# Performance work log

Hardware: AMD Instinct MI355X
Metric: run time of the kernel (lower is better)

Reference implementation:

```python
import jax, jax.numpy as jnp
import numpy as np

N_NODES = 50000
N_EDGES = 800000
D_IN, D_HID, D_OUT = 64, 128, 64


def _graph_conv(x, src, dst, w_rel, w_root, b):
    # PyG GraphConv with aggr='sum':
    #   out_i = W_rel @ sum_{j in N(i)} x_j + W_root @ x_i + b
    # Aggregate first at input width (sum commutes with the linear map),
    # then apply the two linear transforms.
    agg = jax.ops.segment_sum(x[src], dst, num_segments=x.shape[0])  # [N, d_in]
    return agg @ w_rel + x @ w_root + b


def setup_inputs() -> dict:
    key = jax.random.key(0)
    ks = jax.random.split(key, 9)
    x = jax.random.normal(ks[0], (N_NODES, D_IN), dtype=jnp.float32)
    edge_index = jax.random.randint(ks[1], (2, N_EDGES), 0, N_NODES, dtype=jnp.int64)

    def glorot(k, fan_in, fan_out):
        s = jnp.sqrt(2.0 / (fan_in + fan_out)).astype(jnp.float32)
        return jax.random.normal(k, (fan_in, fan_out), dtype=jnp.float32) * s

    return {
        "x": x,
        "edge_index": edge_index,
        "w_rel1": glorot(ks[2], D_IN, D_HID),  "w_root1": glorot(ks[3], D_IN, D_HID),  "b1": jnp.zeros((D_HID,), jnp.float32),
        "w_rel2": glorot(ks[4], D_HID, D_HID), "w_root2": glorot(ks[5], D_HID, D_HID), "b2": jnp.zeros((D_HID,), jnp.float32),
        "w_rel3": glorot(ks[6], D_HID, D_OUT), "w_root3": glorot(ks[7], D_HID, D_OUT), "b3": jnp.zeros((D_OUT,), jnp.float32),
    }


def reference(x, edge_index, w_rel1, w_root1, b1, w_rel2, w_root2, b2, w_rel3, w_root3, b3):
    src, dst = edge_index[0], edge_index[1]
    h = jax.nn.relu(_graph_conv(x, src, dst, w_rel1, w_root1, b1))
    h = jax.nn.relu(_graph_conv(h, src, dst, w_rel2, w_root2, b2))
    out = _graph_conv(h, src, dst, w_rel3, w_root3, b3)  # final layer: no relu
    return out
```

## Files before the change

### kernel.cpp

```cpp
#include <hip/hip_runtime.h>
#include <hip/hip_bf16.h>


#define N_D_IN 64
#define N_D_HID 128
#define N_D_OUT 64

__global__ void detect_kernel(const unsigned int* __restrict__ w, int* __restrict__ flag) {
    __shared__ int nonzero;
    if (threadIdx.x == 0) nonzero = 0;
    __syncthreads();
    for (int i = threadIdx.x; i < 1024; i += 256) {
        if (w[2 * i + 1] != 0u) atomicOr(&nonzero, 1);
    }
    __syncthreads();
    if (threadIdx.x == 0) *flag = (nonzero ? 0 : 1);
}

__device__ __forceinline__ int load_edge(const void* edge, const int* flag, size_t idx) {
    if (*flag) return (int)((const long long*)edge)[idx];
    return ((const int*)edge)[idx];
}

__global__ void hist_kernel(const void* __restrict__ edge, const int* __restrict__ flag,
                            int* __restrict__ cnt, int n_edges) {
    int i = blockIdx.x * 256 + threadIdx.x;
    if (i >= n_edges) return;
    int d = load_edge(edge, flag, (size_t)n_edges + i);
    atomicAdd(&cnt[d], 1);
}

__global__ __launch_bounds__(256) void blocksum_kernel(const int* __restrict__ cnt,
                                                       int* __restrict__ bsum, int n) {
    int i = blockIdx.x * 256 + threadIdx.x;
    int v = (i < n) ? cnt[i] : 0;
#pragma unroll
    for (int off = 1; off < 64; off <<= 1) v += __shfl_xor(v, off);
    __shared__ int wsums[4];
    if ((threadIdx.x & 63) == 0) wsums[threadIdx.x >> 6] = v;
    __syncthreads();
    if (threadIdx.x == 0) bsum[blockIdx.x] = wsums[0] + wsums[1] + wsums[2] + wsums[3];
}

__global__ __launch_bounds__(1024) void scan_bsum_kernel(const int* __restrict__ bsum,
                                                         int* __restrict__ boff, int nb) {
    __shared__ int tmp[1024];
    int t = threadIdx.x;
    int v = (t < nb) ? bsum[t] : 0;
    tmp[t] = v;
    __syncthreads();
    for (int off = 1; off < 1024; off <<= 1) {
        int u = (t >= off) ? tmp[t - off] : 0;
        __syncthreads();
        tmp[t] += u;
        __syncthreads();
    }
    if (t < nb) boff[t] = tmp[t] - v;
}

__global__ __launch_bounds__(256) void emit_kernel(const int* __restrict__ cnt,
                                                   const int* __restrict__ boff,
                                                   int* __restrict__ row_ptr,
                                                   int* __restrict__ cursor, int n) {
    __shared__ int tmp[256];
    int b = blockIdx.x, t = threadIdx.x;
    int i = b * 256 + t;
    int v = (i < n) ? cnt[i] : 0;
    tmp[t] = v;
    __syncthreads();
    for (int off = 1; off < 256; off <<= 1) {
        int u = (t >= off) ? tmp[t - off] : 0;
        __syncthreads();
        tmp[t] += u;
        __syncthreads();
    }
    int excl = tmp[t] - v + boff[b];
    if (i < n) {
        row_ptr[i] = excl;
        cursor[i] = excl;
        if (i == n - 1) row_ptr[n] = excl + v;
    }
}

__global__ void scatter_kernel(const void* __restrict__ edge, const int* __restrict__ flag,
                               int* __restrict__ cursor, int* __restrict__ srcs, int n_edges) {
    int i = blockIdx.x * 256 + threadIdx.x;
    if (i >= n_edges) return;
    int s = load_edge(edge, flag, (size_t)i);
    int d = load_edge(edge, flag, (size_t)n_edges + i);
    int pos = atomicAdd(&cursor[d], 1);
    srcs[pos] = s;
}

template <int D, bool ADD_BASE>
__global__ __launch_bounds__(256) void agg_kernel(const float* __restrict__ in,
                                                  const float* __restrict__ base,
                                                  float* __restrict__ out,
                                                  const int* __restrict__ row_ptr,
                                                  const int* __restrict__ srcs, int n_nodes) {
    constexpr int LPR = D / 4;
    constexpr int SLOTS = 64 / LPR;
    const int node = blockIdx.x * 4 + (threadIdx.x >> 6);
    if (node >= n_nodes) return;
    const int lane = threadIdx.x & 63;
    const int c4 = lane % LPR;
    const int slot = lane / LPR;
    const int e0 = row_ptr[node], e1 = row_ptr[node + 1];
    float4 acc = make_float4(0.f, 0.f, 0.f, 0.f);
    for (int e = e0 + slot; e < e1; e += SLOTS) {
        int s = srcs[e];
        float4 v = *(const float4*)&in[(size_t)s * D + c4 * 4];
        acc.x += v.x; acc.y += v.y; acc.z += v.z; acc.w += v.w;
    }
#pragma unroll
    for (int off = LPR; off < 64; off <<= 1) {
        acc.x += __shfl_xor(acc.x, off);
        acc.y += __shfl_xor(acc.y, off);
        acc.z += __shfl_xor(acc.z, off);
        acc.w += __shfl_xor(acc.w, off);
    }
    if (lane < LPR) {
        if (ADD_BASE) {
            float4 b = *(const float4*)&base[(size_t)node * D + c4 * 4];
            acc.x += b.x; acc.y += b.y; acc.z += b.z; acc.w += b.w;
        }
        *(float4*)&out[(size_t)node * D + c4 * 4] = acc;
    }
}

template <int DIN, int DOUT, int MODE, int TM, bool RELU>
__global__ __launch_bounds__(256) void gemm_tiled(const float* __restrict__ A,
                                                  const float* __restrict__ B,
                                                  const float* __restrict__ W1,
                                                  const float* __restrict__ W2,
                                                  const float* __restrict__ bias,
                                                  float* __restrict__ o1,
                                                  float* __restrict__ o2, int n_nodes) {
    constexpr int KT = 32;
    constexpr int JS = DOUT / 4;
    constexpr int NL = 256 / JS;
    constexpr int BN = NL * TM;
    constexpr int NKT = DIN / KT;
    constexpr int K4T = KT / 4;
    constexpr int W4 = (KT * DOUT / 4) / 256;
    constexpr int AL = (BN * KT / 4) / 256;

    __shared__ float sA[BN][KT];
    __shared__ float sB[(MODE == 1) ? BN : 1][(MODE == 1) ? KT : 4];
    __shared__ float sW1[KT][DOUT];
    __shared__ float sW2[KT][DOUT];

    const int tid = threadIdx.x;
    const int node0 = blockIdx.x * BN;
    const int jslot = tid % JS;
    const int j0 = jslot * 4;
    const int nlane = tid / JS;

    float acc1[TM][4];
    float acc2[(MODE == 2) ? TM : 1][4];
#pragma unroll
    for (int m = 0; m < TM; ++m)
#pragma unroll
        for (int c = 0; c < 4; ++c) {
            acc1[m][c] = 0.f;
            if constexpr (MODE == 2) acc2[m][c] = 0.f;
        }

#pragma unroll 1
    for (int kt = 0; kt < NKT; ++kt) {
#pragma unroll
        for (int r = 0; r < AL; ++r) {
            int idx = r * 256 + tid;
            int n = idx / K4T, c4 = idx % K4T;
            int gn = node0 + n;
            float4 av = make_float4(0.f, 0.f, 0.f, 0.f);
            float4 bv = make_float4(0.f, 0.f, 0.f, 0.f);
            if (gn < n_nodes) {
                av = *(const float4*)&A[(size_t)gn * DIN + kt * KT + c4 * 4];
                if constexpr (MODE == 1)
                    bv = *(const float4*)&B[(size_t)gn * DIN + kt * KT + c4 * 4];
            }
            *(float4*)&sA[n][c4 * 4] = av;
            if constexpr (MODE == 1) *(float4*)&sB[n][c4 * 4] = bv;
        }
#pragma unroll
        for (int w = 0; w < W4; ++w) {
            int idx = w * 256 + tid;
            int r = idx / (DOUT / 4), c4 = idx % (DOUT / 4);
            *(float4*)&sW1[r][c4 * 4] =
                *(const float4*)&W1[(size_t)(kt * KT + r) * DOUT + c4 * 4];
            *(float4*)&sW2[r][c4 * 4] =
                *(const float4*)&W2[(size_t)(kt * KT + r) * DOUT + c4 * 4];
        }
        __syncthreads();

#pragma unroll
        for (int k4 = 0; k4 < K4T; ++k4) {
            float w1s[4][4], w2s[4][4];
#pragma unroll
            for (int u = 0; u < 4; ++u) {
                float4 t = *(const float4*)&sW1[k4 * 4 + u][j0];
                w1s[u][0] = t.x; w1s[u][1] = t.y; w1s[u][2] = t.z; w1s[u][3] = t.w;
                float4 t2 = *(const float4*)&sW2[k4 * 4 + u][j0];
                w2s[u][0] = t2.x; w2s[u][1] = t2.y; w2s[u][2] = t2.z; w2s[u][3] = t2.w;
            }
#pragma unroll
            for (int m = 0; m < TM; ++m) {
                int n = nlane * TM + m;
                float4 a4 = *(const float4*)&sA[n][k4 * 4];
                float av[4] = {a4.x, a4.y, a4.z, a4.w};
                if constexpr (MODE == 1) {
                    float4 b4 = *(const float4*)&sB[n][k4 * 4];
                    float bv4[4] = {b4.x, b4.y, b4.z, b4.w};
#pragma unroll
                    for (int c = 0; c < 4; ++c)
#pragma unroll
                        for (int u = 0; u < 4; ++u)
                            acc1[m][c] += av[u] * w1s[u][c] + bv4[u] * w2s[u][c];
                } else {
#pragma unroll
                    for (int c = 0; c < 4; ++c)
#pragma unroll
                        for (int u = 0; u < 4; ++u) {
                            acc1[m][c] += av[u] * w1s[u][c];
                            acc2[m][c] += av[u] * w2s[u][c];
                        }
                }
            }
        }
        __syncthreads();
    }

    float4 bt = *(const float4*)&bias[j0];
    float bv[4] = {bt.x, bt.y, bt.z, bt.w};
#pragma unroll
    for (int m = 0; m < TM; ++m) {
        int gn = node0 + nlane * TM + m;
        if (gn < n_nodes) {
            if constexpr (MODE == 1) {
                float v0 = acc1[m][0] + bv[0], v1 = acc1[m][1] + bv[1];
                float v2 = acc1[m][2] + bv[2], v3 = acc1[m][3] + bv[3];
                if constexpr (RELU) {
                    v0 = fmaxf(v0, 0.f); v1 = fmaxf(v1, 0.f);
                    v2 = fmaxf(v2, 0.f); v3 = fmaxf(v3, 0.f);
                }
                float4 o; o.x = v0; o.y = v1; o.z = v2; o.w = v3;
                *(float4*)&o1[(size_t)gn * DOUT + j0] = o;
            } else {
                float4 q;
                q.x = acc1[m][0]; q.y = acc1[m][1]; q.z = acc1[m][2]; q.w = acc1[m][3];
                *(float4*)&o1[(size_t)gn * DOUT + j0] = q;
                float4 r;
                r.x = acc2[m][0] + bv[0]; r.y = acc2[m][1] + bv[1];
                r.z = acc2[m][2] + bv[2]; r.w = acc2[m][3] + bv[3];
                *(float4*)&o2[(size_t)gn * DOUT + j0] = r;
            }
        }
    }
}

extern "C" void kernel_launch(void* const* d_in, const int* in_sizes, int n_in,
                              void* d_out, int out_size, void* d_ws, size_t ws_size,
                              hipStream_t stream) {
    const float* x = (const float*)d_in[0];
    const void* edge = d_in[1];
    const float* w_rel1 = (const float*)d_in[2];
    const float* w_root1 = (const float*)d_in[3];
    const float* b1 = (const float*)d_in[4];
    const float* w_rel2 = (const float*)d_in[5];
    const float* w_root2 = (const float*)d_in[6];
    const float* b2 = (const float*)d_in[7];
    const float* w_rel3 = (const float*)d_in[8];
    const float* w_root3 = (const float*)d_in[9];
    const float* b3 = (const float*)d_in[10];
    float* out = (float*)d_out;

    const int n_nodes = in_sizes[0] / N_D_IN;
    const int n_edges = in_sizes[1] / 2;

    char* ws = (char*)d_ws;
    int* cnt = (int*)(ws + 0);
    int* row_ptr = (int*)(ws + (1 << 20));
    int* cursor = (int*)(ws + (2 << 20));
    int* flag = (int*)(ws + (3 << 20));
    int* bsum = (int*)(ws + (3 << 20) + 1024);
    int* boff = (int*)(ws + (3 << 20) + 1024 + 4096);
    int* srcs = (int*)(ws + (4 << 20));
    float* agg = (float*)(ws + (size_t)(8 << 20));
    float* h1 = (float*)(ws + (size_t)(34 << 20));
    float* h2 = (float*)(ws + (size_t)(60 << 20));
    float* t3 = (float*)(ws + (size_t)(34 << 20));
    float* base3 = (float*)(ws + (size_t)(47 << 20));

    const int eblk = (n_edges + 255) / 256;
    const int nblk = (n_nodes + 255) / 256;
    const int ablk = (n_nodes + 3) / 4;
    const int gblk = (n_nodes + 63) / 64;

    hipMemsetAsync(cnt, 0, (size_t)n_nodes * sizeof(int), stream);
    detect_kernel<<<1, 256, 0, stream>>>((const unsigned int*)edge, flag);
    hist_kernel<<<eblk, 256, 0, stream>>>(edge, flag, cnt, n_edges);
    blocksum_kernel<<<nblk, 256, 0, stream>>>(cnt, bsum, n_nodes);
    scan_bsum_kernel<<<1, 1024, 0, stream>>>(bsum, boff, nblk);
    emit_kernel<<<nblk, 256, 0, stream>>>(cnt, boff, row_ptr, cursor, n_nodes);
    scatter_kernel<<<eblk, 256, 0, stream>>>(edge, flag, cursor, srcs, n_edges);

    agg_kernel<64, false><<<ablk, 256, 0, stream>>>(x, nullptr, agg, row_ptr, srcs, n_nodes);
    gemm_tiled<64, 128, 1, 8, true><<<gblk, 256, 0, stream>>>(
        agg, x, w_rel1, w_root1, b1, h1, nullptr, n_nodes);

    agg_kernel<128, false><<<ablk, 256, 0, stream>>>(h1, nullptr, agg, row_ptr, srcs, n_nodes);
    gemm_tiled<128, 128, 1, 8, true><<<gblk, 256, 0, stream>>>(
        agg, h1, w_rel2, w_root2, b2, h2, nullptr, n_nodes);

    gemm_tiled<128, 64, 2, 4, false><<<gblk, 256, 0, stream>>>(
        h2, nullptr, w_rel3, w_root3, b3, t3, base3, n_nodes);
    agg_kernel<64, true><<<ablk, 256, 0, stream>>>(t3, base3, out, row_ptr, srcs, n_nodes);
}
```

Measured before the change: 498.2 us.

## Rewrite dense GEMMs to read weights as wave-uniform scalar loads

Replaces the shared-memory tiled GEMM with a layout where each wave owns a slice of output columns and each lane owns one node row. The weight indices are wave-uniform through readfirstlane, so the compiler can fetch weights with scalar loads instead of staging them in LDS. Only activations go through padded LDS. The cost is fewer rows per thread and more accumulator registers per thread (up to 32 per output), which may lower occupancy and reduce FMA reuse compared with the 8x4 register tile.

```diff
diff --git a/kernel.cpp b/kernel.cpp
--- a/kernel.cpp
+++ b/kernel.cpp
@@ -128,132 +128,121 @@
     }
 }
 
-template <int DIN, int DOUT, int MODE, int TM, bool RELU>
-__global__ __launch_bounds__(256) void gemm_tiled(const float* __restrict__ A,
-                                                  const float* __restrict__ B,
-                                                  const float* __restrict__ W1,
-                                                  const float* __restrict__ W2,
-                                                  const float* __restrict__ bias,
-                                                  float* __restrict__ o1,
-                                                  float* __restrict__ o2, int n_nodes) {
-    constexpr int KT = 32;
-    constexpr int JS = DOUT / 4;
-    constexpr int NL = 256 / JS;
-    constexpr int BN = NL * TM;
+template <int DIN, int DOUT, int MODE, bool RELU>
+__global__ __launch_bounds__(256) void gemm_sgpr(const float* __restrict__ A,
+                                                 const float* __restrict__ B,
+                                                 const float* __restrict__ W1,
+                                                 const float* __restrict__ W2,
+                                                 const float* __restrict__ bias,
+                                                 float* __restrict__ o1,
+                                                 float* __restrict__ o2, int n_nodes) {
+    constexpr int BN = 64;
+    constexpr int KT = 64;
     constexpr int NKT = DIN / KT;
     constexpr int K4T = KT / 4;
-    constexpr int W4 = (KT * DOUT / 4) / 256;
-    constexpr int AL = (BN * KT / 4) / 256;
-
-    __shared__ float sA[BN][KT];
-    __shared__ float sB[(MODE == 1) ? BN : 1][(MODE == 1) ? KT : 4];
-    __shared__ float sW1[KT][DOUT];
-    __shared__ float sW2[KT][DOUT];
+    constexpr int WC = DOUT / 4;
+    constexpr int PAD = 4;
+    constexpr int AL = (BN * (KT / 4)) / 256;
+
+    __shared__ float sA[BN][KT + PAD];
+    __shared__ float sB[(MODE == 1) ? BN : 1][(MODE == 1) ? (KT + PAD) : 4];
 
     const int tid = threadIdx.x;
+    const int lane = tid & 63;
+    const int wv = __builtin_amdgcn_readfirstlane(tid >> 6);
+    const int c0 = wv * WC;
     const int node0 = blockIdx.x * BN;
-    const int jslot = tid % JS;
-    const int j0 = jslot * 4;
-    const int nlane = tid / JS;
-
-    float acc1[TM][4];
-    float acc2[(MODE == 2) ? TM : 1][4];
-#pragma unroll
-    for (int m = 0; m < TM; ++m)
-#pragma unroll
-        for (int c = 0; c < 4; ++c) {
-            acc1[m][c] = 0.f;
-            if constexpr (MODE == 2) acc2[m][c] = 0.f;
-        }
+    const int gn = node0 + lane;
+
+    float acc1[WC];
+    float acc2[(MODE == 2) ? WC : 1];
+#pragma unroll
+    for (int c = 0; c < WC; ++c) {
+        acc1[c] = 0.f;
+        if constexpr (MODE == 2) acc2[c] = 0.f;
+    }
 
 #pragma unroll 1
     for (int kt = 0; kt < NKT; ++kt) {
 #pragma unroll
         for (int r = 0; r < AL; ++r) {
             int idx = r * 256 + tid;
-            int n = idx / K4T, c4 = idx % K4T;
-            int gn = node0 + n;
+            int n = idx / (KT / 4), c4 = idx % (KT / 4);
+            int g = node0 + n;
             float4 av = make_float4(0.f, 0.f, 0.f, 0.f);
             float4 bv = make_float4(0.f, 0.f, 0.f, 0.f);
-            if (gn < n_nodes) {
-                av = *(const float4*)&A[(size_t)gn * DIN + kt * KT + c4 * 4];
+            if (g < n_nodes) {
+                av = *(const float4*)&A[(size_t)g * DIN + kt * KT + c4 * 4];
                 if constexpr (MODE == 1)
-                    bv = *(const float4*)&B[(size_t)gn * DIN + kt * KT + c4 * 4];
+                    bv = *(const float4*)&B[(size_t)g * DIN + kt * KT + c4 * 4];
             }
             *(float4*)&sA[n][c4 * 4] = av;
             if constexpr (MODE == 1) *(float4*)&sB[n][c4 * 4] = bv;
         }
-#pragma unroll
-        for (int w = 0; w < W4; ++w) {
-            int idx = w * 256 + tid;
-            int r = idx / (DOUT / 4), c4 = idx % (DOUT / 4);
-            *(float4*)&sW1[r][c4 * 4] =
-                *(const float4*)&W1[(size_t)(kt * KT + r) * DOUT + c4 * 4];
-            *(float4*)&sW2[r][c4 * 4] =
-                *(const float4*)&W2[(size_t)(kt * KT + r) * DOUT + c4 * 4];
-        }
-        __syncthreads();
-
-#pragma unroll
+        __syncthreads();
+
+#pragma unroll 1
         for (int k4 = 0; k4 < K4T; ++k4) {
-            float w1s[4][4], w2s[4][4];
-#pragma unroll
-            for (int u = 0; u < 4; ++u) {
-                float4 t = *(const float4*)&sW1[k4 * 4 + u][j0];
-                w1s[u][0] = t.x; w1s[u][1] = t.y; w1s[u][2] = t.z; w1s[u][3] = t.w;
-                float4 t2 = *(const float4*)&sW2[k4 * 4 + u][j0];
-                w2s[u][0] = t2.x; w2s[u][1] = t2.y; w2s[u][2] = t2.z; w2s[u][3] = t2.w;
+            float4 a4 = *(const float4*)&sA[lane][k4 * 4];
+            float av[4] = {a4.x, a4.y, a4.z, a4.w};
+            float bvv[4];
+            if constexpr (MODE == 1) {
+                float4 b4 = *(const float4*)&sB[lane][k4 * 4];
+                bvv[0] = b4.x; bvv[1] = b4.y; bvv[2] = b4.z; bvv[3] = b4.w;
             }
-#pragma unroll
-            for (int m = 0; m < TM; ++m) {
-                int n = nlane * TM + m;
-                float4 a4 = *(const float4*)&sA[n][k4 * 4];
-                float av[4] = {a4.x, a4.y, a4.z, a4.w};
-                if constexpr (MODE == 1) {
-                    float4 b4 = *(const float4*)&sB[n][k4 * 4];
-                    float bv4[4] = {b4.x, b4.y, b4.z, b4.w};
-#pragma unroll
-                    for (int c = 0; c < 4; ++c)
-#pragma unroll
-                        for (int u = 0; u < 4; ++u)
-                            acc1[m][c] += av[u] * w1s[u][c] + bv4[u] * w2s[u][c];
-                } else {
-#pragma unroll
-                    for (int c = 0; c < 4; ++c)
-#pragma unroll
-                        for (int u = 0; u < 4; ++u) {
-                            acc1[m][c] += av[u] * w1s[u][c];
-                            acc2[m][c] += av[u] * w2s[u][c];
+            const float* w1p = W1 + (size_t)(kt * KT + k4 * 4) * DOUT + c0;
+            const float* w2p = W2 + (size_t)(kt * KT + k4 * 4) * DOUT + c0;
+#pragma unroll
+            for (int cg = 0; cg < WC / 8; ++cg) {
+                float w1s[4][8], w2s[4][8];
+#pragma unroll
+                for (int u = 0; u < 4; ++u)
+#pragma unroll
+                    for (int c = 0; c < 8; ++c) {
+                        w1s[u][c] = w1p[u * DOUT + cg * 8 + c];
+                        w2s[u][c] = w2p[u * DOUT + cg * 8 + c];
+                    }
+#pragma unroll
+                for (int c = 0; c < 8; ++c)
+#pragma unroll
+                    for (int u = 0; u < 4; ++u) {
+                        if constexpr (MODE == 1) {
+                            acc1[cg * 8 + c] += av[u] * w1s[u][c] + bvv[u] * w2s[u][c];
+                        } else {
+                            acc1[cg * 8 + c] += av[u] * w1s[u][c];
+                            acc2[cg * 8 + c] += av[u] * w2s[u][c];
                         }
-                }
+                    }
             }
         }
         __syncthreads();
     }
 
-    float4 bt = *(const float4*)&bias[j0];
-    float bv[4] = {bt.x, bt.y, bt.z, bt.w};
-#pragma unroll
-    for (int m = 0; m < TM; ++m) {
-        int gn = node0 + nlane * TM + m;
-        if (gn < n_nodes) {
+    if (gn < n_nodes) {
+#pragma unroll
+        for (int cs = 0; cs < WC / 4; ++cs) {
+            float4 o;
             if constexpr (MODE == 1) {
-                float v0 = acc1[m][0] + bv[0], v1 = acc1[m][1] + bv[1];
-                float v2 = acc1[m][2] + bv[2], v3 = acc1[m][3] + bv[3];
+                float b0 = bias[c0 + cs * 4 + 0], b1v = bias[c0 + cs * 4 + 1];
+                float b2v = bias[c0 + cs * 4 + 2], b3v = bias[c0 + cs * 4 + 3];
+                float v0 = acc1[cs * 4 + 0] + b0, v1 = acc1[cs * 4 + 1] + b1v;
+                float v2 = acc1[cs * 4 + 2] + b2v, v3 = acc1[cs * 4 + 3] + b3v;
                 if constexpr (RELU) {
                     v0 = fmaxf(v0, 0.f); v1 = fmaxf(v1, 0.f);
                     v2 = fmaxf(v2, 0.f); v3 = fmaxf(v3, 0.f);
                 }
-                float4 o; o.x = v0; o.y = v1; o.z = v2; o.w = v3;
-                *(float4*)&o1[(size_t)gn * DOUT + j0] = o;
+                o.x = v0; o.y = v1; o.z = v2; o.w = v3;
+                *(float4*)&o1[(size_t)gn * DOUT + c0 + cs * 4] = o;
             } else {
-                float4 q;
-                q.x = acc1[m][0]; q.y = acc1[m][1]; q.z = acc1[m][2]; q.w = acc1[m][3];
-                *(float4*)&o1[(size_t)gn * DOUT + j0] = q;
+                o.x = acc1[cs * 4 + 0]; o.y = acc1[cs * 4 + 1];
+                o.z = acc1[cs * 4 + 2]; o.w = acc1[cs * 4 + 3];
+                *(float4*)&o1[(size_t)gn * DOUT + c0 + cs * 4] = o;
                 float4 r;
-                r.x = acc2[m][0] + bv[0]; r.y = acc2[m][1] + bv[1];
-                r.z = acc2[m][2] + bv[2]; r.w = acc2[m][3] + bv[3];
-                *(float4*)&o2[(size_t)gn * DOUT + j0] = r;
+                r.x = acc2[cs * 4 + 0] + bias[c0 + cs * 4 + 0];
+                r.y = acc2[cs * 4 + 1] + bias[c0 + cs * 4 + 1];
+                r.z = acc2[cs * 4 + 2] + bias[c0 + cs * 4 + 2];
+                r.w = acc2[cs * 4 + 3] + bias[c0 + cs * 4 + 3];
+                *(float4*)&o2[(size_t)gn * DOUT + c0 + cs * 4] = r;
             }
         }
     }
@@ -306,14 +295,14 @@
     scatter_kernel<<<eblk, 256, 0, stream>>>(edge, flag, cursor, srcs, n_edges);
 
     agg_kernel<64, false><<<ablk, 256, 0, stream>>>(x, nullptr, agg, row_ptr, srcs, n_nodes);
-    gemm_tiled<64, 128, 1, 8, true><<<gblk, 256, 0, stream>>>(
+    gemm_sgpr<64, 128, 1, true><<<gblk, 256, 0, stream>>>(
         agg, x, w_rel1, w_root1, b1, h1, nullptr, n_nodes);
 
     agg_kernel<128, false><<<ablk, 256, 0, stream>>>(h1, nullptr, agg, row_ptr, srcs, n_nodes);
-    gemm_tiled<128, 128, 1, 8, true><<<gblk, 256, 0, stream>>>(
+    gemm_sgpr<128, 128, 1, true><<<gblk, 256, 0, stream>>>(
         agg, h1, w_rel2, w_root2, b2, h2, nullptr, n_nodes);
 
-    gemm_tiled<128, 64, 2, 4, false><<<gblk, 256, 0, stream>>>(
+    gemm_sgpr<128, 64, 2, false><<<gblk, 256, 0, stream>>>(
         h2, nullptr, w_rel3, w_root3, b3, t3, base3, n_nodes);
     agg_kernel<64, true><<<ablk, 256, 0, stream>>>(t3, base3, out, row_ptr, srcs, n_nodes);
 }
```

Result: slower. 701.0 us (+40.7%).
